# Optimization experiments

Hardware: AMD Instinct MI355X
Metric: run time of the kernel (lower is better)

Reference implementation:

```python
import jax, jax.numpy as jnp
import numpy as np
from jax import lax

B, V, C, D, H, W = 1, 5, 32, 48, 128, 160
RATIO = 8


def setup_inputs() -> dict:
    key = jax.random.key(0)
    k1, k2, k3 = jax.random.split(key, 3)
    features = jax.random.normal(k1, (V, B, C, H, W), jnp.float32)
    # proj_matrices[b, v, 0] = 4x4 extrinsic, proj_matrices[b, v, 1, :3, :3] = intrinsic K
    f = 200.0
    K = np.array([[f, 0.0, W / 2.0], [0.0, f, H / 2.0], [0.0, 0.0, 1.0]], np.float32)
    proj = np.zeros((B, V, 2, 4, 4), np.float32)
    for v in range(V):
        E = np.eye(4, dtype=np.float32)
        E[0, 3] = 2.0 * v  # horizontal baseline per source view
        proj[:, v, 0] = E
        P1 = np.eye(4, dtype=np.float32)
        P1[:3, :3] = K
        proj[:, v, 1] = P1
    proj_matrices = jnp.asarray(proj)
    depth_values = jnp.broadcast_to(jnp.linspace(425.0, 935.0, D, dtype=jnp.float32), (B, D))
    mask = jax.random.normal(k2, (B, 9 * RATIO * RATIO, H, W), jnp.float32)
    W_reg = jax.random.normal(k3, (1, C, 3, 3, 3), jnp.float32) * 0.05
    return {"features": features, "proj_matrices": proj_matrices,
            "depth_values": depth_values, "mask": mask, "W_reg": W_reg}


def _combine(p):
    # p: [B,2,4,4] -> K @ E[:3,:4] written into top 3 rows of extrinsic (as in source)
    top = jnp.einsum('bij,bjk->bik', p[:, 1, :3, :3], p[:, 0, :3, :4])
    return p[:, 0].at[:, :3, :4].set(top)


def _bilinear_sample(src, x, y):
    # src [B,C,H,W]; x,y [B,P] pixel coords; zeros padding, align_corners=True
    Bs, Cs, Hs, Ws = src.shape
    x0 = jnp.floor(x)
    y0 = jnp.floor(y)
    wx = x - x0
    wy = y - y0
    src_flat = src.reshape(Bs, Cs, Hs * Ws)

    def gather(xi, yi, w):
        valid = (xi >= 0) & (xi <= Ws - 1) & (yi >= 0) & (yi <= Hs - 1)
        xi_c = jnp.clip(xi, 0, Ws - 1).astype(jnp.int32)
        yi_c = jnp.clip(yi, 0, Hs - 1).astype(jnp.int32)
        idx = (yi_c * Ws + xi_c)[:, None, :]
        vals = jnp.take_along_axis(src_flat, jnp.broadcast_to(idx, (Bs, Cs, idx.shape[-1])), axis=2)
        return vals * (w * valid)[:, None, :]

    return (gather(x0, y0, (1 - wx) * (1 - wy)) + gather(x0 + 1, y0, wx * (1 - wy))
            + gather(x0, y0 + 1, (1 - wx) * wy) + gather(x0 + 1, y0 + 1, wx * wy))


def _homo_warp(src_fea, src_proj, ref_proj, depth_values):
    # faithful homo_warping2: project ref pixel grid at each depth hypothesis into src view
    Bs, Cs, Hs, Ws = src_fea.shape
    Dd = depth_values.shape[1]
    proj = jnp.einsum('bij,bjk->bik', src_proj, jnp.linalg.inv(ref_proj))
    rot = proj[:, :3, :3]
    trans = proj[:, :3, 3]
    ys, xs = jnp.meshgrid(jnp.arange(Hs, dtype=src_fea.dtype), jnp.arange(Ws, dtype=src_fea.dtype), indexing='ij')
    xyz = jnp.stack([xs.ravel(), ys.ravel(), jnp.ones(Hs * Ws, dtype=src_fea.dtype)])  # [3,HW]
    rot_xyz = jnp.einsum('bij,jp->bip', rot, xyz)  # [B,3,HW]
    pts = rot_xyz[:, :, None, :] * depth_values[:, None, :, None] + trans[:, :, None, None]  # [B,3,D,HW]
    gx = pts[:, 0] / pts[:, 2]
    gy = pts[:, 1] / pts[:, 2]
    warped = _bilinear_sample(src_fea, gx.reshape(Bs, -1), gy.reshape(Bs, -1))
    return warped.reshape(Bs, Cs, Dd, Hs, Ws)


def _convex_upsample(depth, mask, r):
    # depth [N,1,H,W], mask [N,9*r*r,H,W] -> [N, r*H, r*W]
    N, _, Hh, Ww = depth.shape
    m = jax.nn.softmax(mask.reshape(N, 1, 9, r, r, Hh, Ww), axis=2)
    dp = jnp.pad(depth, ((0, 0), (0, 0), (1, 1), (1, 1)))
    nb = jnp.stack([dp[:, :, dy:dy + Hh, dx:dx + Ww] for dy in range(3) for dx in range(3)], axis=2)
    up = jnp.sum(m * nb[:, :, :, None, None], axis=2)  # [N,1,r,r,H,W]
    up = up.transpose(0, 1, 4, 2, 5, 3)  # [N,1,H,r,W,r]
    return up.reshape(N, r * Hh, r * Ww)


def reference(features, proj_matrices, depth_values, mask, W_reg):
    num_views = features.shape[0]
    Dd = depth_values.shape[1]
    ref_proj = _combine(proj_matrices[:, 0])
    # variance cost-volume accumulation over views (ref volume broadcast along D)
    vsum = features[0][:, :, None, :, :]
    vsq = vsum ** 2
    for v in range(1, num_views):
        src_proj = _combine(proj_matrices[:, v])
        wv = _homo_warp(features[v], src_proj, ref_proj, depth_values)
        vsum = vsum + wv
        vsq = vsq + wv * wv
    variance = vsq / num_views - (vsum / num_views) ** 2  # [B,C,D,H,W]
    # cost regularization stand-in: 3x3x3 conv C->1, SAME padding
    pre = lax.conv_general_dilated(variance, W_reg, (1, 1, 1), 'SAME',
                                   dimension_numbers=('NCDHW', 'OIDHW', 'NCDHW'))[:, 0]
    prob = jax.nn.softmax(pre, axis=1)  # [B,D,H,W]
    depth = jnp.sum(prob * depth_values[:, :, None, None], axis=1)  # [B,H,W]
    # photometric confidence (no-grad path): sliding sum of 4 along D, pad (1,2)
    pd = jnp.pad(prob, ((0, 0), (1, 2), (0, 0), (0, 0)))
    sum4 = pd[:, 0:Dd] + pd[:, 1:Dd + 1] + pd[:, 2:Dd + 2] + pd[:, 3:Dd + 3]
    di = jnp.sum(prob * jnp.arange(Dd, dtype=prob.dtype)[None, :, None, None], axis=1).astype(jnp.int32)
    di = jnp.clip(di, 0, Dd - 1)
    conf = jax.lax.stop_gradient(jnp.take_along_axis(sum4, di[:, None], axis=1)[:, 0])
    depth_up = _convex_upsample(depth[:, None], mask, RATIO)
    return (depth_up, depth, conf)
```

## Files before the change

kernel.cpp:

```cpp
#include <hip/hip_runtime.h>
#include <hip/hip_bf16.h>


#define NV 5
#define NC 32
#define ND 48
#define NH 128
#define NW 160
#define HW (NH * NW)
#define DHW (ND * HW)

typedef __attribute__((ext_vector_type(2))) float f32x2;

#define OFF_M      0
#define OFF_WF     256
#define OFF_DEPTHF 4096
#define OFF_PRE    86016
#define OFF_WV     4018176

__global__ void k_setup(const float* __restrict__ proj,
                        const float* __restrict__ wreg,
                        float* __restrict__ M, float* __restrict__ wf) {
  if (threadIdx.x != 0) return;
  double P[NV][2][4][4];
  for (int v = 0; v < NV; ++v)
    for (int m = 0; m < 2; ++m)
      for (int i = 0; i < 4; ++i)
        for (int j = 0; j < 4; ++j)
          P[v][m][i][j] = (double)proj[((v * 2 + m) * 4 + i) * 4 + j];
  double C[NV][4][4];
  for (int v = 0; v < NV; ++v) {
    for (int i = 0; i < 4; ++i)
      for (int j = 0; j < 4; ++j) C[v][i][j] = P[v][0][i][j];
    for (int i = 0; i < 3; ++i)
      for (int j = 0; j < 4; ++j) {
        double s = 0.0;
        for (int k = 0; k < 3; ++k) s += P[v][1][i][k] * P[v][0][k][j];
        C[v][i][j] = s;
      }
  }
  double a[4][8];
  for (int i = 0; i < 4; ++i)
    for (int j = 0; j < 4; ++j) { a[i][j] = C[0][i][j]; a[i][j + 4] = (i == j) ? 1.0 : 0.0; }
  for (int col = 0; col < 4; ++col) {
    int piv = col; double best = fabs(a[col][col]);
    for (int r = col + 1; r < 4; ++r) { double v = fabs(a[r][col]); if (v > best) { best = v; piv = r; } }
    if (piv != col)
      for (int j = 0; j < 8; ++j) { double t = a[col][j]; a[col][j] = a[piv][j]; a[piv][j] = t; }
    double pv = a[col][col];
    for (int j = 0; j < 8; ++j) a[col][j] /= pv;
    for (int r = 0; r < 4; ++r) if (r != col) {
      double f = a[r][col];
      for (int j = 0; j < 8; ++j) a[r][j] -= f * a[col][j];
    }
  }
  double inv[4][4];
  for (int i = 0; i < 4; ++i)
    for (int j = 0; j < 4; ++j) inv[i][j] = a[i][j + 4];
  for (int v = 1; v < NV; ++v) {
    float* m = M + (v - 1) * 12;
    for (int i = 0; i < 3; ++i) {
      double r[4] = {0, 0, 0, 0};
      for (int k = 0; k < 4; ++k) {
        double cv = C[v][i][k];
        for (int j = 0; j < 4; ++j) r[j] += cv * inv[k][j];
      }
      m[i * 3 + 0] = (float)r[0]; m[i * 3 + 1] = (float)r[1]; m[i * 3 + 2] = (float)r[2];
      m[9 + i] = (float)r[3];
    }
  }
  for (int c = 0; c < NC; ++c) {
    for (int t = 0; t < 27; ++t) wf[c * 28 + t] = wreg[c * 27 + t];
    wf[c * 28 + 27] = 0.f;
  }
}

__global__ __launch_bounds__(256) void k_warpvar(
    const float* __restrict__ feat,
    const float* __restrict__ depthv,
    const float* __restrict__ M,
    const float* __restrict__ wf,
    __hip_bfloat16* __restrict__ WV)
{
  int idx = blockIdx.x * 256 + threadIdx.x;
  int x = idx % NW;
  int t1 = idx / NW;
  int y = t1 % NH;
  int d = t1 / NH;
  float xf = (float)x, yf = (float)y;
  float df = depthv[d];

  int   cidx[16];
  float cw[16];
#pragma unroll
  for (int v = 0; v < 4; ++v) {
    const float* m = M + v * 12;
    float rx = m[0] * xf + m[1] * yf + m[2];
    float ry = m[3] * xf + m[4] * yf + m[5];
    float rz = m[6] * xf + m[7] * yf + m[8];
    float px = rx * df + m[9];
    float py = ry * df + m[10];
    float pz = rz * df + m[11];
    float gx = px / pz;
    float gy = py / pz;
    float x0 = floorf(gx), y0 = floorf(gy);
    float wx = gx - x0, wy = gy - y0;
    float cxs[2] = {x0, x0 + 1.f}, cys[2] = {y0, y0 + 1.f};
    float wxs[2] = {1.f - wx, wx}, wys[2] = {1.f - wy, wy};
#pragma unroll
    for (int cy = 0; cy < 2; ++cy)
#pragma unroll
      for (int cx = 0; cx < 2; ++cx) {
        float fx = cxs[cx], fy = cys[cy];
        bool valid = (fx >= 0.f) && (fx <= (float)(NW - 1)) &&
                     (fy >= 0.f) && (fy <= (float)(NH - 1));
        float fxc = fminf(fmaxf(fx, 0.f), (float)(NW - 1));
        float fyc = fminf(fmaxf(fy, 0.f), (float)(NH - 1));
        int xi = (int)fxc, yi = (int)fyc;
        cidx[v * 4 + cy * 2 + cx] = yi * NW + xi;
        cw[v * 4 + cy * 2 + cx] = wxs[cx] * wys[cy] * (valid ? 1.f : 0.f);
      }
  }

  int pix = y * NW + x;
  f32x2 wv[14];
#pragma unroll
  for (int u = 0; u < 14; ++u) wv[u] = (f32x2){0.f, 0.f};

#pragma unroll
  for (int c = 0; c < NC; ++c) {
    float f0 = feat[c * HW + pix];
    float vs = f0, vq = f0 * f0;
#pragma unroll
    for (int v = 0; v < 4; ++v) {
      const float* fv = feat + ((v + 1) * NC + c) * HW;
      float val = cw[v * 4 + 0] * fv[cidx[v * 4 + 0]]
                + cw[v * 4 + 1] * fv[cidx[v * 4 + 1]]
                + cw[v * 4 + 2] * fv[cidx[v * 4 + 2]]
                + cw[v * 4 + 3] * fv[cidx[v * 4 + 3]];
      vs += val;
      vq += val * val;
    }
    float var = vq * 0.2f - (vs * 0.2f) * (vs * 0.2f);
    const f32x2* wrow = (const f32x2*)(wf + c * 28);
    f32x2 vv; vv.x = var; vv.y = var;
#pragma unroll
    for (int u = 0; u < 14; ++u) wv[u] += wrow[u] * vv;
  }

#pragma unroll
  for (int u = 0; u < 14; ++u) {
    int t0 = 2 * u;
    WV[t0 * DHW + idx] = __float2bfloat16(wv[u].x);
    if (t0 + 1 < 27) WV[(t0 + 1) * DHW + idx] = __float2bfloat16(wv[u].y);
  }
}

__global__ __launch_bounds__(256) void k_conv(const __hip_bfloat16* __restrict__ WV,
                                              float* __restrict__ pre) {
  int idx = blockIdx.x * 256 + threadIdx.x;
  int x = idx % NW;
  int t1 = idx / NW;
  int y = t1 % NH;
  int d = t1 / NH;
  float acc = 0.f;
#pragma unroll
  for (int dd = 0; dd < 3; ++dd) {
    int dp = d + dd - 1;
    bool dok = (dp >= 0) && (dp < ND);
    int dpc = min(max(dp, 0), ND - 1);
#pragma unroll
    for (int i = 0; i < 3; ++i) {
      int yp = y + i - 1;
      bool yok = (yp >= 0) && (yp < NH);
      int ypc = min(max(yp, 0), NH - 1);
#pragma unroll
      for (int j = 0; j < 3; ++j) {
        int xp = x + j - 1;
        bool xok = (xp >= 0) && (xp < NW);
        int xpc = min(max(xp, 0), NW - 1);
        int t = dd * 9 + i * 3 + j;
        float v = __bfloat162float(WV[t * DHW + dpc * HW + ypc * NW + xpc]);
        acc += (dok && yok && xok) ? v : 0.f;
      }
    }
  }
  pre[idx] = acc;
}

__global__ __launch_bounds__(256) void k_softmax(const float* __restrict__ pre,
                                                 const float* __restrict__ depthv,
                                                 float* __restrict__ depthf,
                                                 float* __restrict__ out_depth,
                                                 float* __restrict__ out_conf) {
  int p = blockIdx.x * 256 + threadIdx.x;
  float pr[ND];
  float m = -1e30f;
#pragma unroll
  for (int d = 0; d < ND; ++d) { pr[d] = pre[d * HW + p]; m = fmaxf(m, pr[d]); }
  float s = 0.f;
#pragma unroll
  for (int d = 0; d < ND; ++d) { pr[d] = expf(pr[d] - m); s += pr[d]; }
  float inv = 1.f / s;
  float dep = 0.f, ti = 0.f;
#pragma unroll
  for (int d = 0; d < ND; ++d) {
    float prob = pr[d] * inv;
    pr[d] = prob;
    dep += prob * depthv[d];
    ti += prob * (float)d;
  }
  int di = (int)ti;
  di = di < 0 ? 0 : (di > ND - 1 ? ND - 1 : di);
  float conf = 0.f;
#pragma unroll
  for (int d = 0; d < ND; ++d)
    conf += (d >= di - 1 && d <= di + 2) ? pr[d] : 0.f;
  depthf[p] = dep;
  out_depth[p] = dep;
  out_conf[p] = conf;
}

__global__ __launch_bounds__(256) void k_upsample(const float* __restrict__ mask,
                                                  const float* __restrict__ depthf,
                                                  float* __restrict__ out) {
  int idx = blockIdx.x * 256 + threadIdx.x;
  int fx = idx % (NW * 8);
  int fy = idx / (NW * 8);
  int x = fx >> 3, dx = fx & 7;
  int y = fy >> 3, dy = fy & 7;
  float mv[9];
  float mmax = -1e30f;
#pragma unroll
  for (int k = 0; k < 9; ++k) {
    mv[k] = mask[((k * 8 + dy) * 8 + dx) * HW + y * NW + x];
    mmax = fmaxf(mmax, mv[k]);
  }
  float s = 0.f;
#pragma unroll
  for (int k = 0; k < 9; ++k) { mv[k] = expf(mv[k] - mmax); s += mv[k]; }
  float acc = 0.f;
#pragma unroll
  for (int k = 0; k < 9; ++k) {
    int ky = y + k / 3 - 1;
    int kx = x + k % 3 - 1;
    bool ok = (ky >= 0) && (ky < NH) && (kx >= 0) && (kx < NW);
    int kyc = min(max(ky, 0), NH - 1);
    int kxc = min(max(kx, 0), NW - 1);
    float dv = depthf[kyc * NW + kxc];
    acc += mv[k] * (ok ? dv : 0.f);
  }
  out[idx] = acc / s;
}

extern "C" void kernel_launch(void* const* d_in, const int* in_sizes, int n_in,
                              void* d_out, int out_size, void* d_ws, size_t ws_size,
                              hipStream_t stream) {
  const float* feat   = (const float*)d_in[0];
  const float* proj   = (const float*)d_in[1];
  const float* depthv = (const float*)d_in[2];
  const float* mask   = (const float*)d_in[3];
  const float* wreg   = (const float*)d_in[4];

  char* ws = (char*)d_ws;
  float* M       = (float*)(ws + OFF_M);
  float* wf      = (float*)(ws + OFF_WF);
  float* depthf  = (float*)(ws + OFF_DEPTHF);
  float* pre     = (float*)(ws + OFF_PRE);
  __hip_bfloat16* WV = (__hip_bfloat16*)(ws + OFF_WV);

  float* out = (float*)d_out;
  float* out_depth = out + (NH * 8) * (NW * 8);
  float* out_conf  = out_depth + HW;

  k_setup<<<1, 64, 0, stream>>>(proj, wreg, M, wf);
  k_warpvar<<<DHW / 256, 256, 0, stream>>>(feat, depthv, M, wf, WV);
  k_conv<<<DHW / 256, 256, 0, stream>>>(WV, pre);
  k_softmax<<<HW / 256, 256, 0, stream>>>(pre, depthv, depthf, out_depth, out_conf);
  k_upsample<<<(NH * 8 * NW * 8) / 256, 256, 0, stream>>>(mask, depthf, out);
}
```

Before: 270.9 us.

## Transpose features to channel-last and add a two-tap path for integer-row samples

A new transpose kernel rewrites the features into a pixel-major, channel-contiguous layout. Each bilinear tap in the warp/variance kernel can then fetch all 32 channels with 16-byte vector loads, instead of 32 separate strided gathers. The warp kernel also checks at runtime whether every view's vertical sampling fraction is zero, and if so evaluates only the two horizontal taps. The cost is an extra kernel pass that writes about 13 MB, plus a workspace region that is reused by the later pre buffer.

```diff
diff --git a/kernel.cpp b/kernel.cpp
--- a/kernel.cpp
+++ b/kernel.cpp
@@ -11,12 +11,14 @@
 #define DHW (ND * HW)
 
 typedef __attribute__((ext_vector_type(2))) float f32x2;
+typedef __attribute__((ext_vector_type(4))) float f32x4;
 
 #define OFF_M      0
 #define OFF_WF     256
 #define OFF_DEPTHF 4096
+#define OFF_FEATT  86016
 #define OFF_PRE    86016
-#define OFF_WV     4018176
+#define OFF_WV     13193216
 
 __global__ void k_setup(const float* __restrict__ proj,
                         const float* __restrict__ wreg,
@@ -75,8 +77,80 @@
   }
 }
 
+__global__ __launch_bounds__(256) void k_transpose(const float* __restrict__ feat,
+                                                   float* __restrict__ featT) {
+  int t = blockIdx.x * 256 + threadIdx.x;
+  int v = t / HW;
+  int pix = t - v * HW;
+  float r[NC];
+#pragma unroll
+  for (int c = 0; c < NC; ++c) r[c] = feat[(v * NC + c) * HW + pix];
+  f32x4* dst = (f32x4*)(featT + (size_t)t * NC);
+#pragma unroll
+  for (int k = 0; k < 8; ++k) {
+    f32x4 o;
+    o.x = r[4 * k + 0]; o.y = r[4 * k + 1]; o.z = r[4 * k + 2]; o.w = r[4 * k + 3];
+    dst[k] = o;
+  }
+}
+
+template <int T>
+__device__ __forceinline__ void warp_accum(
+    const char* __restrict__ refp,
+    const char* const* tb,
+    const float* tw,
+    const float* __restrict__ wf,
+    __hip_bfloat16* __restrict__ WV, int idx)
+{
+  f32x2 wv[14];
+#pragma unroll
+  for (int u = 0; u < 14; ++u) { wv[u].x = 0.f; wv[u].y = 0.f; }
+
+#pragma unroll
+  for (int k = 0; k < 8; ++k) {
+    f32x4 vs = *(const f32x4*)(refp + k * 16);
+    f32x4 vq;
+    vq.x = vs.x * vs.x; vq.y = vs.y * vs.y; vq.z = vs.z * vs.z; vq.w = vs.w * vs.w;
+#pragma unroll
+    for (int v = 0; v < 4; ++v) {
+      f32x4 val; val.x = 0.f; val.y = 0.f; val.z = 0.f; val.w = 0.f;
+#pragma unroll
+      for (int t = 0; t < T; ++t) {
+        f32x4 f = *(const f32x4*)(tb[v * T + t] + k * 16);
+        float w = tw[v * T + t];
+        val.x += f.x * w; val.y += f.y * w; val.z += f.z * w; val.w += f.w * w;
+      }
+      vs.x += val.x; vs.y += val.y; vs.z += val.z; vs.w += val.w;
+      vq.x += val.x * val.x; vq.y += val.y * val.y;
+      vq.z += val.z * val.z; vq.w += val.w * val.w;
+    }
+    f32x4 var;
+    var.x = vq.x * 0.2f - (vs.x * 0.2f) * (vs.x * 0.2f);
+    var.y = vq.y * 0.2f - (vs.y * 0.2f) * (vs.y * 0.2f);
+    var.z = vq.z * 0.2f - (vs.z * 0.2f) * (vs.z * 0.2f);
+    var.w = vq.w * 0.2f - (vs.w * 0.2f) * (vs.w * 0.2f);
+#pragma unroll
+    for (int ch = 0; ch < 4; ++ch) {
+      float vv = var[ch];
+      const f32x2* wrow = (const f32x2*)(wf + (k * 4 + ch) * 28);
+#pragma unroll
+      for (int u = 0; u < 14; ++u) {
+        wv[u].x += wrow[u].x * vv;
+        wv[u].y += wrow[u].y * vv;
+      }
+    }
+  }
+
+#pragma unroll
+  for (int u = 0; u < 14; ++u) {
+    int t0 = 2 * u;
+    WV[t0 * DHW + idx] = __float2bfloat16(wv[u].x);
+    if (t0 + 1 < 27) WV[(t0 + 1) * DHW + idx] = __float2bfloat16(wv[u].y);
+  }
+}
+
 __global__ __launch_bounds__(256) void k_warpvar(
-    const float* __restrict__ feat,
+    const float* __restrict__ featT,
     const float* __restrict__ depthv,
     const float* __restrict__ M,
     const float* __restrict__ wf,
@@ -90,8 +164,9 @@
   float xf = (float)x, yf = (float)y;
   float df = depthv[d];
 
-  int   cidx[16];
-  float cw[16];
+  const char* tb4[16];
+  float tw4[16];
+  bool all2 = true;
 #pragma unroll
   for (int v = 0; v < 4; ++v) {
     const float* m = M + v * 12;
@@ -105,8 +180,10 @@
     float gy = py / pz;
     float x0 = floorf(gx), y0 = floorf(gy);
     float wx = gx - x0, wy = gy - y0;
+    all2 = all2 && (wy == 0.f);
     float cxs[2] = {x0, x0 + 1.f}, cys[2] = {y0, y0 + 1.f};
     float wxs[2] = {1.f - wx, wx}, wys[2] = {1.f - wy, wy};
+    const char* vbase = (const char*)featT + (size_t)(v + 1) * HW * (NC * 4);
 #pragma unroll
     for (int cy = 0; cy < 2; ++cy)
 #pragma unroll
@@ -117,42 +194,24 @@
         float fxc = fminf(fmaxf(fx, 0.f), (float)(NW - 1));
         float fyc = fminf(fmaxf(fy, 0.f), (float)(NH - 1));
         int xi = (int)fxc, yi = (int)fyc;
-        cidx[v * 4 + cy * 2 + cx] = yi * NW + xi;
-        cw[v * 4 + cy * 2 + cx] = wxs[cx] * wys[cy] * (valid ? 1.f : 0.f);
-      }
-  }
-
+        tb4[v * 4 + cy * 2 + cx] = vbase + (size_t)(yi * NW + xi) * (NC * 4);
+        tw4[v * 4 + cy * 2 + cx] = wxs[cx] * wys[cy] * (valid ? 1.f : 0.f);
+      }
+  }
   int pix = y * NW + x;
-  f32x2 wv[14];
-#pragma unroll
-  for (int u = 0; u < 14; ++u) wv[u] = (f32x2){0.f, 0.f};
-
-#pragma unroll
-  for (int c = 0; c < NC; ++c) {
-    float f0 = feat[c * HW + pix];
-    float vs = f0, vq = f0 * f0;
+  const char* refp = (const char*)featT + (size_t)pix * (NC * 4);
+
+  if (all2) {
+    const char* tb2[8];
+    float tw2[8];
 #pragma unroll
     for (int v = 0; v < 4; ++v) {
-      const float* fv = feat + ((v + 1) * NC + c) * HW;
-      float val = cw[v * 4 + 0] * fv[cidx[v * 4 + 0]]
-                + cw[v * 4 + 1] * fv[cidx[v * 4 + 1]]
-                + cw[v * 4 + 2] * fv[cidx[v * 4 + 2]]
-                + cw[v * 4 + 3] * fv[cidx[v * 4 + 3]];
-      vs += val;
-      vq += val * val;
-    }
-    float var = vq * 0.2f - (vs * 0.2f) * (vs * 0.2f);
-    const f32x2* wrow = (const f32x2*)(wf + c * 28);
-    f32x2 vv; vv.x = var; vv.y = var;
-#pragma unroll
-    for (int u = 0; u < 14; ++u) wv[u] += wrow[u] * vv;
-  }
-
-#pragma unroll
-  for (int u = 0; u < 14; ++u) {
-    int t0 = 2 * u;
-    WV[t0 * DHW + idx] = __float2bfloat16(wv[u].x);
-    if (t0 + 1 < 27) WV[(t0 + 1) * DHW + idx] = __float2bfloat16(wv[u].y);
+      tb2[v * 2 + 0] = tb4[v * 4 + 0]; tw2[v * 2 + 0] = tw4[v * 4 + 0];
+      tb2[v * 2 + 1] = tb4[v * 4 + 1]; tw2[v * 2 + 1] = tw4[v * 4 + 1];
+    }
+    warp_accum<2>(refp, tb2, tw2, wf, WV, idx);
+  } else {
+    warp_accum<4>(refp, tb4, tw4, wf, WV, idx);
   }
 }
 
@@ -266,6 +325,7 @@
   float* M       = (float*)(ws + OFF_M);
   float* wf      = (float*)(ws + OFF_WF);
   float* depthf  = (float*)(ws + OFF_DEPTHF);
+  float* featT   = (float*)(ws + OFF_FEATT);
   float* pre     = (float*)(ws + OFF_PRE);
   __hip_bfloat16* WV = (__hip_bfloat16*)(ws + OFF_WV);
 
@@ -274,7 +334,8 @@
   float* out_conf  = out_depth + HW;
 
   k_setup<<<1, 64, 0, stream>>>(proj, wreg, M, wf);
-  k_warpvar<<<DHW / 256, 256, 0, stream>>>(feat, depthv, M, wf, WV);
+  k_transpose<<<(NV * HW) / 256, 256, 0, stream>>>(feat, featT);
+  k_warpvar<<<DHW / 256, 256, 0, stream>>>(featT, depthv, M, wf, WV);
   k_conv<<<DHW / 256, 256, 0, stream>>>(WV, pre);
   k_softmax<<<HW / 256, 256, 0, stream>>>(pre, depthv, depthf, out_depth, out_conf);
   k_upsample<<<(NH * 8 * NW * 8) / 256, 256, 0, stream>>>(mask, depthf, out);
```

Measured after the change: 490.4 us. 1.81x slower.

## Process two pixels per thread with a row-aligned two-tap warp fast path

Applied to the files above, without the earlier changes.

The warp-variance kernel now handles two adjacent pixels per thread. When every view's sample row is integer-aligned (vertical fraction exactly 0 or 1), it uses a two-tap horizontal path. That path fetches both taps with one unaligned 8-byte load per view and skips the zero-weight row. Otherwise it falls back to the full four-tap bilinear path per pixel. It also packs the two bf16 outputs into 32-bit stores. This cuts gather loads and index math, at the cost of higher register pressure (27 float2 accumulators), a divergent fallback branch and half as many threads.

```diff
diff --git a/kernel.cpp b/kernel.cpp
--- a/kernel.cpp
+++ b/kernel.cpp
@@ -11,12 +11,21 @@
 #define DHW (ND * HW)
 
 typedef __attribute__((ext_vector_type(2))) float f32x2;
+typedef __attribute__((ext_vector_type(2), aligned(4))) float f32x2u;
 
 #define OFF_M      0
 #define OFF_WF     256
 #define OFF_DEPTHF 4096
 #define OFF_PRE    86016
 #define OFF_WV     4018176
+
+__device__ __forceinline__ uint32_t pack_bf16(float a, float b) {
+  __hip_bfloat16 ba = __float2bfloat16(a), bb = __float2bfloat16(b);
+  uint16_t ua, ub;
+  __builtin_memcpy(&ua, &ba, 2);
+  __builtin_memcpy(&ub, &bb, 2);
+  return (uint32_t)ua | ((uint32_t)ub << 16);
+}
 
 __global__ void k_setup(const float* __restrict__ proj,
                         const float* __restrict__ wreg,
@@ -80,80 +89,173 @@
     const float* __restrict__ depthv,
     const float* __restrict__ M,
     const float* __restrict__ wf,
-    __hip_bfloat16* __restrict__ WV)
+    uint32_t* __restrict__ WV2)
 {
-  int idx = blockIdx.x * 256 + threadIdx.x;
-  int x = idx % NW;
-  int t1 = idx / NW;
+  int t = blockIdx.x * 256 + threadIdx.x;
+  int idx0 = t * 2;
+  int x = idx0 % NW;
+  int t1 = idx0 / NW;
   int y = t1 % NH;
   int d = t1 / NH;
-  float xf = (float)x, yf = (float)y;
+  int pix = y * NW + x;
+  float yf = (float)y;
   float df = depthv[d];
 
-  int   cidx[16];
-  float cw[16];
+  int offA[4], offB[4];
+  int sA[4], sB[4], dA[4], dB[4];
+  float w0A[4], w1A[4], w0B[4], w1B[4];
+  bool any4 = false;
+
 #pragma unroll
   for (int v = 0; v < 4; ++v) {
     const float* m = M + v * 12;
-    float rx = m[0] * xf + m[1] * yf + m[2];
-    float ry = m[3] * xf + m[4] * yf + m[5];
-    float rz = m[6] * xf + m[7] * yf + m[8];
-    float px = rx * df + m[9];
-    float py = ry * df + m[10];
-    float pz = rz * df + m[11];
-    float gx = px / pz;
-    float gy = py / pz;
-    float x0 = floorf(gx), y0 = floorf(gy);
-    float wx = gx - x0, wy = gy - y0;
-    float cxs[2] = {x0, x0 + 1.f}, cys[2] = {y0, y0 + 1.f};
-    float wxs[2] = {1.f - wx, wx}, wys[2] = {1.f - wy, wy};
-#pragma unroll
-    for (int cy = 0; cy < 2; ++cy)
-#pragma unroll
-      for (int cx = 0; cx < 2; ++cx) {
-        float fx = cxs[cx], fy = cys[cy];
-        bool valid = (fx >= 0.f) && (fx <= (float)(NW - 1)) &&
-                     (fy >= 0.f) && (fy <= (float)(NH - 1));
-        float fxc = fminf(fmaxf(fx, 0.f), (float)(NW - 1));
-        float fyc = fminf(fmaxf(fy, 0.f), (float)(NH - 1));
-        int xi = (int)fxc, yi = (int)fyc;
-        cidx[v * 4 + cy * 2 + cx] = yi * NW + xi;
-        cw[v * 4 + cy * 2 + cx] = wxs[cx] * wys[cy] * (valid ? 1.f : 0.f);
-      }
-  }
-
-  int pix = y * NW + x;
-  f32x2 wv[14];
-#pragma unroll
-  for (int u = 0; u < 14; ++u) wv[u] = (f32x2){0.f, 0.f};
-
-#pragma unroll
+    int offs[2], ss[2], dds[2];
+    float w0s[2], w1s[2];
+#pragma unroll
+    for (int j = 0; j < 2; ++j) {
+      float xf = (float)(x + j);
+      float rx = m[0] * xf + m[1] * yf + m[2];
+      float ry = m[3] * xf + m[4] * yf + m[5];
+      float rz = m[6] * xf + m[7] * yf + m[8];
+      float px = rx * df + m[9];
+      float py = ry * df + m[10];
+      float pz = rz * df + m[11];
+      float gx = px / pz;
+      float gy = py / pz;
+      float y0 = floorf(gy);
+      float wy = gy - y0;
+      bool two = (wy == 0.f) || (wy == 1.f);
+      any4 = any4 || !two;
+      float rowf = (wy == 0.f) ? y0 : (y0 + 1.f);
+      float x0 = floorf(gx);
+      float wx = gx - x0;
+      bool yok  = (rowf >= 0.f) && (rowf <= (float)(NH - 1));
+      bool x0ok = (x0 >= 0.f) && (x0 <= (float)(NW - 1)) && yok;
+      bool x1ok = (x0 + 1.f >= 0.f) && (x0 + 1.f <= (float)(NW - 1)) && yok;
+      float rc = fminf(fmaxf(rowf, 0.f), (float)(NH - 1));
+      float xc = fminf(fmaxf(x0, 0.f), (float)(NW - 1));
+      int xi = (int)xc;
+      int off = (int)rc * NW + xi;
+      int s  = (xi <= NW - 2) ? 1 : 0;
+      int dd = (off == HW - 1) ? 1 : 0;
+      offs[j] = off - dd;
+      ss[j] = s; dds[j] = dd;
+      w0s[j] = (1.f - wx) * (x0ok ? 1.f : 0.f);
+      w1s[j] = wx * (x1ok ? 1.f : 0.f);
+    }
+    offA[v] = offs[0]; offB[v] = offs[1];
+    sA[v] = ss[0]; sB[v] = ss[1];
+    dA[v] = dds[0]; dB[v] = dds[1];
+    w0A[v] = w0s[0]; w1A[v] = w1s[0];
+    w0B[v] = w0s[1]; w1B[v] = w1s[1];
+  }
+
+  if (any4) {
+    f32x2 acc[27];
+#pragma unroll
+    for (int u = 0; u < 27; ++u) { acc[u].x = 0.f; acc[u].y = 0.f; }
+#pragma unroll
+    for (int j = 0; j < 2; ++j) {
+      float xf = (float)(x + j);
+      int cidx[16]; float cw[16];
+#pragma unroll
+      for (int v = 0; v < 4; ++v) {
+        const float* m = M + v * 12;
+        float rx = m[0] * xf + m[1] * yf + m[2];
+        float ry = m[3] * xf + m[4] * yf + m[5];
+        float rz = m[6] * xf + m[7] * yf + m[8];
+        float px = rx * df + m[9];
+        float py = ry * df + m[10];
+        float pz = rz * df + m[11];
+        float gx = px / pz;
+        float gy = py / pz;
+        float x0 = floorf(gx), y0 = floorf(gy);
+        float wx = gx - x0, wy = gy - y0;
+        float cxs[2] = {x0, x0 + 1.f}, cys[2] = {y0, y0 + 1.f};
+        float wxs[2] = {1.f - wx, wx}, wys[2] = {1.f - wy, wy};
+#pragma unroll
+        for (int cy = 0; cy < 2; ++cy)
+#pragma unroll
+          for (int cx = 0; cx < 2; ++cx) {
+            float fx = cxs[cx], fy = cys[cy];
+            bool valid = (fx >= 0.f) && (fx <= (float)(NW - 1)) &&
+                         (fy >= 0.f) && (fy <= (float)(NH - 1));
+            float fxc = fminf(fmaxf(fx, 0.f), (float)(NW - 1));
+            float fyc = fminf(fmaxf(fy, 0.f), (float)(NH - 1));
+            int xi2 = (int)fxc, yi2 = (int)fyc;
+            cidx[v * 4 + cy * 2 + cx] = yi2 * NW + xi2;
+            cw[v * 4 + cy * 2 + cx] = wxs[cx] * wys[cy] * (valid ? 1.f : 0.f);
+          }
+      }
+      int pj = pix + j;
+#pragma unroll 4
+      for (int c = 0; c < NC; ++c) {
+        float f0 = feat[c * HW + pj];
+        float vsS = f0, vqS = f0 * f0;
+#pragma unroll
+        for (int v = 0; v < 4; ++v) {
+          const float* fv = feat + ((v + 1) * NC + c) * HW;
+          float val = cw[v * 4 + 0] * fv[cidx[v * 4 + 0]]
+                    + cw[v * 4 + 1] * fv[cidx[v * 4 + 1]]
+                    + cw[v * 4 + 2] * fv[cidx[v * 4 + 2]]
+                    + cw[v * 4 + 3] * fv[cidx[v * 4 + 3]];
+          vsS += val;
+          vqS += val * val;
+        }
+        float var = vqS * 0.2f - (vsS * 0.2f) * (vsS * 0.2f);
+        const float* wrow = wf + c * 28;
+#pragma unroll
+        for (int u = 0; u < 27; ++u) {
+          if (j == 0) acc[u].x += wrow[u] * var;
+          else        acc[u].y += wrow[u] * var;
+        }
+      }
+    }
+#pragma unroll
+    for (int u = 0; u < 27; ++u)
+      WV2[(size_t)u * (DHW / 2) + t] = pack_bf16(acc[u].x, acc[u].y);
+    return;
+  }
+
+  f32x2 wv2[27];
+#pragma unroll
+  for (int u = 0; u < 27; ++u) { wv2[u].x = 0.f; wv2[u].y = 0.f; }
+
+#pragma unroll 4
   for (int c = 0; c < NC; ++c) {
-    float f0 = feat[c * HW + pix];
-    float vs = f0, vq = f0 * f0;
+    const float* fc = feat + c * HW;
+    f32x2 r2 = *(const f32x2*)(fc + pix);
+    f32x2 vs = r2;
+    f32x2 vq = r2 * r2;
 #pragma unroll
     for (int v = 0; v < 4; ++v) {
       const float* fv = feat + ((v + 1) * NC + c) * HW;
-      float val = cw[v * 4 + 0] * fv[cidx[v * 4 + 0]]
-                + cw[v * 4 + 1] * fv[cidx[v * 4 + 1]]
-                + cw[v * 4 + 2] * fv[cidx[v * 4 + 2]]
-                + cw[v * 4 + 3] * fv[cidx[v * 4 + 3]];
-      vs += val;
-      vq += val * val;
-    }
-    float var = vq * 0.2f - (vs * 0.2f) * (vs * 0.2f);
-    const f32x2* wrow = (const f32x2*)(wf + c * 28);
-    f32x2 vv; vv.x = var; vv.y = var;
-#pragma unroll
-    for (int u = 0; u < 14; ++u) wv[u] += wrow[u] * vv;
-  }
-
-#pragma unroll
-  for (int u = 0; u < 14; ++u) {
-    int t0 = 2 * u;
-    WV[t0 * DHW + idx] = __float2bfloat16(wv[u].x);
-    if (t0 + 1 < 27) WV[(t0 + 1) * DHW + idx] = __float2bfloat16(wv[u].y);
-  }
+      f32x2u ea = *(const f32x2u*)(fv + offA[v]);
+      f32x2u eb = *(const f32x2u*)(fv + offB[v]);
+      float a0 = dA[v] ? ea.y : ea.x;
+      float a1 = sA[v] ? ea.y : a0;
+      float b0 = dB[v] ? eb.y : eb.x;
+      float b1 = sB[v] ? eb.y : b0;
+      float vx = w0A[v] * a0 + w1A[v] * a1;
+      float vy = w0B[v] * b0 + w1B[v] * b1;
+      vs.x += vx; vs.y += vy;
+      vq.x += vx * vx; vq.y += vy * vy;
+    }
+    f32x2 var;
+    var.x = vq.x * 0.2f - (vs.x * 0.2f) * (vs.x * 0.2f);
+    var.y = vq.y * 0.2f - (vs.y * 0.2f) * (vs.y * 0.2f);
+    const float* wrow = wf + c * 28;
+#pragma unroll
+    for (int u = 0; u < 27; ++u) {
+      float w = wrow[u];
+      wv2[u].x += w * var.x;
+      wv2[u].y += w * var.y;
+    }
+  }
+
+#pragma unroll
+  for (int u = 0; u < 27; ++u)
+    WV2[(size_t)u * (DHW / 2) + t] = pack_bf16(wv2[u].x, wv2[u].y);
 }
 
 __global__ __launch_bounds__(256) void k_conv(const __hip_bfloat16* __restrict__ WV,
@@ -267,14 +369,15 @@
   float* wf      = (float*)(ws + OFF_WF);
   float* depthf  = (float*)(ws + OFF_DEPTHF);
   float* pre     = (float*)(ws + OFF_PRE);
-  __hip_bfloat16* WV = (__hip_bfloat16*)(ws + OFF_WV);
+  uint32_t* WV2  = (uint32_t*)(ws + OFF_WV);
+  const __hip_bfloat16* WV = (const __hip_bfloat16*)(ws + OFF_WV);
 
   float* out = (float*)d_out;
   float* out_depth = out + (NH * 8) * (NW * 8);
   float* out_conf  = out_depth + HW;
 
   k_setup<<<1, 64, 0, stream>>>(proj, wreg, M, wf);
-  k_warpvar<<<DHW / 256, 256, 0, stream>>>(feat, depthv, M, wf, WV);
+  k_warpvar<<<(DHW / 2) / 256, 256, 0, stream>>>(feat, depthv, M, wf, WV2);
   k_conv<<<DHW / 256, 256, 0, stream>>>(WV, pre);
   k_softmax<<<HW / 256, 256, 0, stream>>>(pre, depthv, depthf, out_depth, out_conf);
   k_upsample<<<(NH * 8 * NW * 8) / 256, 256, 0, stream>>>(mask, depthf, out);
```

Measured after the change: 330.9 us. +22.1%, slower.

## Use two-tap row sampling when warp is row-aligned; restructure upsample per 8 outputs

Applied to the files above, without the earlier changes.

The warp-variance kernel now checks whether every source view's sample lands exactly on a pixel row (fractional y of 0 or 1). When it does, it reads one unaligned float pair per view instead of four scattered gathers, with border cases folded into the two weights. Otherwise it falls back to the original four-tap path. The upsample kernel now has each thread produce 8 horizontally adjacent outputs, reusing the 9 depth neighbours and writing two float4 stores, which cuts redundant depth loads and index arithmetic. The fast path only applies when the geometry is row-aligned, as with the horizontal-baseline test cameras, and adds branch divergence and register pressure from the duplicated code.

```diff
diff --git a/kernel.cpp b/kernel.cpp
--- a/kernel.cpp
+++ b/kernel.cpp
@@ -11,6 +11,8 @@
 #define DHW (ND * HW)
 
 typedef __attribute__((ext_vector_type(2))) float f32x2;
+typedef __attribute__((ext_vector_type(4))) float f32x4;
+typedef __attribute__((ext_vector_type(2), aligned(4))) float f32x2u;
 
 #define OFF_M      0
 #define OFF_WF     256
@@ -87,11 +89,14 @@
   int t1 = idx / NW;
   int y = t1 % NH;
   int d = t1 / NH;
+  int pix = y * NW + x;
   float xf = (float)x, yf = (float)y;
   float df = depthv[d];
 
-  int   cidx[16];
-  float cw[16];
+  int   off[4];
+  float wA[4], wB[4];
+  bool any4 = false;
+
 #pragma unroll
   for (int v = 0; v < 4; ++v) {
     const float* m = M + v * 12;
@@ -103,49 +108,104 @@
     float pz = rz * df + m[11];
     float gx = px / pz;
     float gy = py / pz;
-    float x0 = floorf(gx), y0 = floorf(gy);
-    float wx = gx - x0, wy = gy - y0;
-    float cxs[2] = {x0, x0 + 1.f}, cys[2] = {y0, y0 + 1.f};
-    float wxs[2] = {1.f - wx, wx}, wys[2] = {1.f - wy, wy};
-#pragma unroll
-    for (int cy = 0; cy < 2; ++cy)
-#pragma unroll
-      for (int cx = 0; cx < 2; ++cx) {
-        float fx = cxs[cx], fy = cys[cy];
-        bool valid = (fx >= 0.f) && (fx <= (float)(NW - 1)) &&
-                     (fy >= 0.f) && (fy <= (float)(NH - 1));
-        float fxc = fminf(fmaxf(fx, 0.f), (float)(NW - 1));
-        float fyc = fminf(fmaxf(fy, 0.f), (float)(NH - 1));
-        int xi = (int)fxc, yi = (int)fyc;
-        cidx[v * 4 + cy * 2 + cx] = yi * NW + xi;
-        cw[v * 4 + cy * 2 + cx] = wxs[cx] * wys[cy] * (valid ? 1.f : 0.f);
-      }
-  }
-
-  int pix = y * NW + x;
+    float y0 = floorf(gy);
+    float wy = gy - y0;
+    bool two = (wy == 0.f) || (wy == 1.f);
+    any4 = any4 || !two;
+    float rowf = (wy == 0.f) ? y0 : (y0 + 1.f);
+    float x0 = floorf(gx);
+    float wx = gx - x0;
+    bool yok  = (rowf >= 0.f) && (rowf <= (float)(NH - 1));
+    bool x0ok = (x0 >= 0.f) && (x0 <= (float)(NW - 1)) && yok;
+    bool x1ok = (x0 + 1.f >= 0.f) && (x0 + 1.f <= (float)(NW - 1)) && yok;
+    float rc = fminf(fmaxf(rowf, 0.f), (float)(NH - 1));
+    float xc = fminf(fmaxf(x0, 0.f), (float)(NW - 1));
+    int xi = (int)xc;
+    int o = (int)rc * NW + xi;
+    bool ddv = (o == HW - 1);
+    bool sv  = (x0 >= 0.f) && (xi <= NW - 2);
+    o -= ddv ? 1 : 0;
+    float w0 = (1.f - wx) * (x0ok ? 1.f : 0.f);
+    float w1 = wx * (x1ok ? 1.f : 0.f);
+    float wsum = w0 + w1;
+    wA[v] = ddv ? 0.f : (sv ? w0 : wsum);
+    wB[v] = ddv ? wsum : (sv ? w1 : 0.f);
+    off[v] = o;
+  }
+
   f32x2 wv[14];
 #pragma unroll
-  for (int u = 0; u < 14; ++u) wv[u] = (f32x2){0.f, 0.f};
-
-#pragma unroll
-  for (int c = 0; c < NC; ++c) {
-    float f0 = feat[c * HW + pix];
-    float vs = f0, vq = f0 * f0;
+  for (int u = 0; u < 14; ++u) { wv[u].x = 0.f; wv[u].y = 0.f; }
+
+  if (__builtin_expect(any4, 0)) {
+    int cidx[16]; float cw[16];
 #pragma unroll
     for (int v = 0; v < 4; ++v) {
-      const float* fv = feat + ((v + 1) * NC + c) * HW;
-      float val = cw[v * 4 + 0] * fv[cidx[v * 4 + 0]]
-                + cw[v * 4 + 1] * fv[cidx[v * 4 + 1]]
-                + cw[v * 4 + 2] * fv[cidx[v * 4 + 2]]
-                + cw[v * 4 + 3] * fv[cidx[v * 4 + 3]];
-      vs += val;
-      vq += val * val;
-    }
-    float var = vq * 0.2f - (vs * 0.2f) * (vs * 0.2f);
-    const f32x2* wrow = (const f32x2*)(wf + c * 28);
-    f32x2 vv; vv.x = var; vv.y = var;
-#pragma unroll
-    for (int u = 0; u < 14; ++u) wv[u] += wrow[u] * vv;
+      const float* m = M + v * 12;
+      float rx = m[0] * xf + m[1] * yf + m[2];
+      float ry = m[3] * xf + m[4] * yf + m[5];
+      float rz = m[6] * xf + m[7] * yf + m[8];
+      float px = rx * df + m[9];
+      float py = ry * df + m[10];
+      float pz = rz * df + m[11];
+      float gx = px / pz;
+      float gy = py / pz;
+      float x0 = floorf(gx), y0 = floorf(gy);
+      float wx = gx - x0, wy = gy - y0;
+      float cxs[2] = {x0, x0 + 1.f}, cys[2] = {y0, y0 + 1.f};
+      float wxs[2] = {1.f - wx, wx}, wys[2] = {1.f - wy, wy};
+#pragma unroll
+      for (int cy = 0; cy < 2; ++cy)
+#pragma unroll
+        for (int cx = 0; cx < 2; ++cx) {
+          float fx = cxs[cx], fy = cys[cy];
+          bool valid = (fx >= 0.f) && (fx <= (float)(NW - 1)) &&
+                       (fy >= 0.f) && (fy <= (float)(NH - 1));
+          float fxc = fminf(fmaxf(fx, 0.f), (float)(NW - 1));
+          float fyc = fminf(fmaxf(fy, 0.f), (float)(NH - 1));
+          int xi2 = (int)fxc, yi2 = (int)fyc;
+          cidx[v * 4 + cy * 2 + cx] = yi2 * NW + xi2;
+          cw[v * 4 + cy * 2 + cx] = wxs[cx] * wys[cy] * (valid ? 1.f : 0.f);
+        }
+    }
+    for (int c = 0; c < NC; ++c) {
+      float f0 = feat[c * HW + pix];
+      float vs = f0, vq = f0 * f0;
+#pragma unroll
+      for (int v = 0; v < 4; ++v) {
+        const float* fv = feat + ((v + 1) * NC + c) * HW;
+        float val = cw[v * 4 + 0] * fv[cidx[v * 4 + 0]]
+                  + cw[v * 4 + 1] * fv[cidx[v * 4 + 1]]
+                  + cw[v * 4 + 2] * fv[cidx[v * 4 + 2]]
+                  + cw[v * 4 + 3] * fv[cidx[v * 4 + 3]];
+        vs += val;
+        vq += val * val;
+      }
+      float var = vq * 0.2f - (vs * 0.2f) * (vs * 0.2f);
+      const f32x2* wrow = (const f32x2*)(wf + c * 28);
+      f32x2 vv; vv.x = var; vv.y = var;
+#pragma unroll
+      for (int u = 0; u < 14; ++u) wv[u] += wrow[u] * vv;
+    }
+  } else {
+#pragma unroll
+    for (int c = 0; c < NC; ++c) {
+      float f0 = feat[c * HW + pix];
+      float vs = f0, vq = f0 * f0;
+#pragma unroll
+      for (int v = 0; v < 4; ++v) {
+        const float* fv = feat + ((v + 1) * NC + c) * HW;
+        f32x2u e = *(const f32x2u*)(fv + off[v]);
+        float val = wA[v] * e.x + wB[v] * e.y;
+        vs += val;
+        vq += val * val;
+      }
+      float var = vq * 0.2f - (vs * 0.2f) * (vs * 0.2f);
+      const f32x2* wrow = (const f32x2*)(wf + c * 28);
+      f32x2 vv; vv.x = var; vv.y = var;
+#pragma unroll
+      for (int u = 0; u < 14; ++u) wv[u] += wrow[u] * vv;
+    }
   }
 
 #pragma unroll
@@ -225,21 +285,13 @@
                                                   const float* __restrict__ depthf,
                                                   float* __restrict__ out) {
   int idx = blockIdx.x * 256 + threadIdx.x;
-  int fx = idx % (NW * 8);
-  int fy = idx / (NW * 8);
-  int x = fx >> 3, dx = fx & 7;
-  int y = fy >> 3, dy = fy & 7;
-  float mv[9];
-  float mmax = -1e30f;
-#pragma unroll
-  for (int k = 0; k < 9; ++k) {
-    mv[k] = mask[((k * 8 + dy) * 8 + dx) * HW + y * NW + x];
-    mmax = fmaxf(mmax, mv[k]);
-  }
-  float s = 0.f;
-#pragma unroll
-  for (int k = 0; k < 9; ++k) { mv[k] = expf(mv[k] - mmax); s += mv[k]; }
-  float acc = 0.f;
+  int x = idx % NW;
+  int r = idx / NW;
+  int y = r % NH;
+  int dy = r / NH;
+  int pix = y * NW + x;
+
+  float dv[9];
 #pragma unroll
   for (int k = 0; k < 9; ++k) {
     int ky = y + k / 3 - 1;
@@ -247,10 +299,36 @@
     bool ok = (ky >= 0) && (ky < NH) && (kx >= 0) && (kx < NW);
     int kyc = min(max(ky, 0), NH - 1);
     int kxc = min(max(kx, 0), NW - 1);
-    float dv = depthf[kyc * NW + kxc];
-    acc += mv[k] * (ok ? dv : 0.f);
-  }
-  out[idx] = acc / s;
+    float t = depthf[kyc * NW + kxc];
+    dv[k] = ok ? t : 0.f;
+  }
+
+  float res[8];
+#pragma unroll
+  for (int dx = 0; dx < 8; ++dx) {
+    float mv[9];
+    float mmax = -1e30f;
+#pragma unroll
+    for (int k = 0; k < 9; ++k) {
+      mv[k] = mask[(size_t)(k * 64 + dy * 8 + dx) * HW + pix];
+      mmax = fmaxf(mmax, mv[k]);
+    }
+    float s = 0.f, acc = 0.f;
+#pragma unroll
+    for (int k = 0; k < 9; ++k) {
+      float e = expf(mv[k] - mmax);
+      s += e;
+      acc += e * dv[k];
+    }
+    res[dx] = acc / s;
+  }
+
+  float* op = out + (size_t)(y * 8 + dy) * (NW * 8) + x * 8;
+  f32x4 lo, hi;
+  lo.x = res[0]; lo.y = res[1]; lo.z = res[2]; lo.w = res[3];
+  hi.x = res[4]; hi.y = res[5]; hi.z = res[6]; hi.w = res[7];
+  *(f32x4*)op = lo;
+  *(f32x4*)(op + 4) = hi;
 }
 
 extern "C" void kernel_launch(void* const* d_in, const int* in_sizes, int n_in,
@@ -277,5 +355,5 @@
   k_warpvar<<<DHW / 256, 256, 0, stream>>>(feat, depthv, M, wf, WV);
   k_conv<<<DHW / 256, 256, 0, stream>>>(WV, pre);
   k_softmax<<<HW / 256, 256, 0, stream>>>(pre, depthv, depthf, out_depth, out_conf);
-  k_upsample<<<(NH * 8 * NW * 8) / 256, 256, 0, stream>>>(mask, depthf, out);
-}
+  k_upsample<<<(NH * 8 * NW * 8 / 8) / 256, 256, 0, stream>>>(mask, depthf, out);
+}
```

Result: faster. 241.3 us (-10.9%).
